# Kernel optimization log

Hardware: AMD Instinct MI355X
Metric: run time of the kernel (lower is better)

The kernel has to match this reference:

```python
import jax, jax.numpy as jnp
import numpy as np

NEAR = 0.2          # near-plane cull, matches uvd[...,2] >= 0.2 in the source
SIGMA2_MAX = 9.0    # 3-sigma disk extent, matches get_disks' sigma3 corners
ALPHA_MIN = 1.0 / 255.0


def quat_to_rot(q):
    """Unit-quaternion [P,4] (w,x,y,z) -> rotation matrices [P,3,3]."""
    q = q / (jnp.linalg.norm(q, axis=-1, keepdims=True) + 1e-12)
    w, x, y, z = q[..., 0], q[..., 1], q[..., 2], q[..., 3]
    r0 = jnp.stack([1 - 2 * (y * y + z * z), 2 * (x * y - w * z), 2 * (x * z + w * y)], -1)
    r1 = jnp.stack([2 * (x * y + w * z), 1 - 2 * (x * x + z * z), 2 * (y * z - w * x)], -1)
    r2 = jnp.stack([2 * (x * z - w * y), 2 * (y * z + w * x), 1 - 2 * (x * x + y * y)], -1)
    return jnp.stack([r0, r1, r2], -2)


def setup_inputs() -> dict:
    key = jax.random.key(0)
    k = jax.random.split(key, 6)
    H = W = 128
    P = 4096
    tanfov = 0.4
    f = W / (2.0 * tanfov)
    xs = (jnp.arange(W, dtype=jnp.float32) - (W - 1) / 2.0) / f
    ys = (jnp.arange(H, dtype=jnp.float32) - (H - 1) / 2.0) / f
    gx, gy = jnp.meshgrid(xs, ys, indexing='xy')
    d = jnp.stack([gx, gy, jnp.ones_like(gx)], -1)
    ray_d = d / jnp.linalg.norm(d, axis=-1, keepdims=True)   # [H,W,3]
    ray_o = jnp.zeros((H, W, 3), jnp.float32)
    means3D = jax.random.normal(k[0], (P, 3), jnp.float32) * 1.5 + jnp.array([0.0, 0.0, 4.0], jnp.float32)
    scales = jax.random.uniform(k[1], (P, 2), jnp.float32, 0.02, 0.15)
    rotations = jax.random.normal(k[2], (P, 4), jnp.float32)
    opacities = jax.random.uniform(k[3], (P, 1), jnp.float32, 0.3, 1.0)
    colors = jax.random.uniform(k[4], (P, 3), jnp.float32)
    bg_color = jnp.zeros((3,), jnp.float32)
    return dict(ray_o=ray_o, ray_d=ray_d, means3D=means3D, scales=scales,
                rotations=rotations, opacities=opacities, colors=colors, bg_color=bg_color)


def reference(ray_o, ray_d, means3D, scales, rotations, opacities, colors, bg_color):
    """Gaussian-surfel ray tracing: ray/disk-plane intersection, 2D Gaussian
    falloff in the surfel tangent frame, front-to-back alpha compositing in
    depth order (the math the BVH-accelerated SurfelTracer computes)."""
    H, W, _ = ray_o.shape
    ro = ray_o.reshape(-1, 3)
    rd = ray_d.reshape(-1, 3)
    R = quat_to_rot(rotations)                     # [P,3,3]
    tu, tv, nrm = R[..., :, 0], R[..., :, 1], R[..., :, 2]  # tangent frame columns

    # ray-plane intersection t = dot(mu - o, n) / dot(d, n)  -> [Nr,P]
    den = rd @ nrm.T
    num = jnp.einsum('pk,pk->p', means3D, nrm)[None, :] - ro @ nrm.T
    safe_den = jnp.where(jnp.abs(den) < 1e-8, 1e-8, den)
    t = num / safe_den

    # local disk coords u,v of hit point without materializing [Nr,P,3]
    u = (ro @ tu.T - jnp.einsum('pk,pk->p', means3D, tu)[None, :] + t * (rd @ tu.T)) / scales[None, :, 0]
    v = (ro @ tv.T - jnp.einsum('pk,pk->p', means3D, tv)[None, :] + t * (rd @ tv.T)) / scales[None, :, 1]
    r2 = u * u + v * v
    G = jnp.exp(-0.5 * r2)
    alpha = jnp.clip(opacities[None, :, 0] * G, 0.0, 0.99)
    valid = (t > NEAR) & (r2 < SIGMA2_MAX) & (jnp.abs(den) > 1e-8) & (alpha > ALPHA_MIN)
    alpha = jnp.where(valid, alpha, 0.0)

    # front-to-back compositing: sort hits by depth per ray
    t_key = jnp.where(valid, t, jnp.inf)
    order = jnp.argsort(t_key, axis=1)
    alpha_s = jnp.take_along_axis(alpha, order, axis=1)
    trans = jnp.cumprod(1.0 - alpha_s, axis=1)
    trans = jnp.concatenate([jnp.ones_like(trans[:, :1]), trans[:, :-1]], axis=1)  # exclusive
    w_s = alpha_s * trans
    inv = jnp.argsort(order, axis=1)
    w = jnp.take_along_axis(w_s, inv, axis=1)      # weights in original surfel order

    acc = w.sum(-1)                                # [Nr]
    rgb = w @ colors + (1.0 - acc)[:, None] * bg_color[None, :]
    dpt = (w * jnp.where(valid, t, 0.0)).sum(-1)
    norm = w @ nrm
    return (rgb.reshape(H, W, 3), dpt.reshape(H, W, 1),
            acc.reshape(H, W, 1), norm.reshape(H, W, 3))
```

## Files before the change

kernel.cpp:

```cpp
#include <hip/hip_runtime.h>
#include <stdint.h>

#define NEAR_T  0.2f
#define SIG2MAX 9.0f
#define AMIN    (1.0f/255.0f)
#define NSL     8
#define TS      8
#define TB      16
#define KFIX    64

__device__ __forceinline__ float dot3(float ax,float ay,float az,
                                      float bx,float by,float bz){
  return fmaf(ax,bx, fmaf(ay,by, az*bz));
}

__device__ __forceinline__ bool eval_hit(const float* __restrict__ gp,
    float rox,float roy,float roz, float rdx,float rdy,float rdz,
    float& t_out, float& a_out)
{
  float nx=gp[6], ny=gp[7], nz=gp[8];
  float den  = dot3(rdx,rdy,rdz, nx,ny,nz);
  float aden = fabsf(den);
  float num  = gp[11] - dot3(rox,roy,roz, nx,ny,nz);
  float sden = (aden < 1e-8f) ? 1e-8f : den;
  float t = __fdividef(num, sden);
  float ru = dot3(rox,roy,roz, gp[0],gp[1],gp[2]);
  float du = dot3(rdx,rdy,rdz, gp[0],gp[1],gp[2]);
  float u  = fmaf(t, du, ru - gp[9])  * gp[12];
  float rv = dot3(rox,roy,roz, gp[3],gp[4],gp[5]);
  float dv = dot3(rdx,rdy,rdz, gp[3],gp[4],gp[5]);
  float v  = fmaf(t, dv, rv - gp[10]) * gp[13];
  float r2 = fmaf(u,u, v*v);
  float G  = __expf(-0.5f*r2);
  float a  = fminf(gp[14]*G, 0.99f);
  t_out = t; a_out = a;
  return (t > NEAR_T) & (r2 < SIG2MAX) & (aden > 1e-8f) & (a > AMIN);
}

__device__ __forceinline__ unsigned long long make_key(float t, float a, uint32_t g){
  uint32_t a16 = (uint32_t)(a * 65535.f + 0.5f);
  return ((unsigned long long)__float_as_uint(t) << 32) |
         ((unsigned long long)a16 << 16) | (unsigned long long)g;
}

__device__ __forceinline__ bool pix_bbox_vals(
    float mx, float my, float mz, float ex, float ey, float ez,
    float axm, float bxm, float aym, float bym, int W, int H,
    int& x0, int& x1, int& y0, int& y1)
{
  float zmin=mz-ez, zmax=mz+ez;
  if (zmax <= 0.16f) return false;
  if (zmin <= 1e-3f){ x0=0; x1=W-1; y0=0; y1=H-1; return true; }
  float xmin=mx-ex, xmax=mx+ex, ymin=my-ey, ymax=my+ey;
  float gxmin = (xmin>=0.f)? xmin/zmax : xmin/zmin;
  float gxmax = (xmax>=0.f)? xmax/zmin : xmax/zmax;
  float gymin = (ymin>=0.f)? ymin/zmax : ymin/zmin;
  float gymax = (ymax>=0.f)? ymax/zmin : ymax/zmax;
  float p0 = (gxmin - bxm)/axm, p1 = (gxmax - bxm)/axm;
  float q0 = (gymin - bym)/aym, q1 = (gymax - bym)/aym;
  int ix0 = (int)floorf(fminf(p0,p1)) - 1;
  int ix1 = (int)ceilf (fmaxf(p0,p1)) + 1;
  int iy0 = (int)floorf(fminf(q0,q1)) - 1;
  int iy1 = (int)ceilf (fmaxf(q0,q1)) + 1;
  if (ix1 < 0 || ix0 > W-1 || iy1 < 0 || iy0 > H-1) return false;
  x0 = max(ix0,0); x1 = min(ix1,W-1);
  y0 = max(iy0,0); y1 = min(iy1,H-1);
  return true;
}

__global__ __launch_bounds__(256)
void k_prep(const float* __restrict__ rot, const float* __restrict__ means,
            const float* __restrict__ scales, const float* __restrict__ opac,
            const float* __restrict__ colors, const float* __restrict__ ray_o,
            const float* __restrict__ ray_d,
            float* __restrict__ geo, float* __restrict__ col,
            int4* __restrict__ bbox, uint32_t* __restrict__ cnt,
            uint32_t* __restrict__ badArr, int P, int npix, int W, int H)
{
  __shared__ int sBad;
  int lt = threadIdx.x;
  if (lt == 0) sBad = 0;
  __syncthreads();
  int tid = blockIdx.x*blockDim.x + lt;
  float g0x = ray_d[0]/ray_d[2], g0y = ray_d[1]/ray_d[2];
  float axm = ray_d[3]/ray_d[5] - g0x;
  float aym = ray_d[(size_t)W*3+1]/ray_d[(size_t)W*3+2] - g0y;
  bool mapok = (fabsf(axm) > 1e-12f) && (fabsf(aym) > 1e-12f);
  if (!mapok) sBad = 1;
  if (tid < npix){
    cnt[tid] = 0u;
    int ix = tid % W, iy = tid / W;
    float rox=ray_o[tid*3+0], roy=ray_o[tid*3+1], roz=ray_o[tid*3+2];
    float rdx=ray_d[tid*3+0], rdy=ray_d[tid*3+1], rdz=ray_d[tid*3+2];
    bool ok = (rox==0.f) & (roy==0.f) & (roz==0.f) & (rdz > 0.8f);
    if (ok && mapok){
      float gx = rdx/rdz, gy = rdy/rdz;
      ok = (fabsf(gx - fmaf(axm,(float)ix,g0x)) <= 3e-4f) &
           (fabsf(gy - fmaf(aym,(float)iy,g0y)) <= 3e-4f);
    }
    if (!ok) sBad = 1;
  }
  if (tid < P){
    int g = tid;
    float qw=rot[g*4+0], qx=rot[g*4+1], qy=rot[g*4+2], qz=rot[g*4+3];
    float n = sqrtf(qw*qw+qx*qx+qy*qy+qz*qz) + 1e-12f;
    qw/=n; qx/=n; qy/=n; qz/=n;
    float tux = 1.f-2.f*(qy*qy+qz*qz), tuy = 2.f*(qx*qy+qw*qz), tuz = 2.f*(qx*qz-qw*qy);
    float tvx = 2.f*(qx*qy-qw*qz), tvy = 1.f-2.f*(qx*qx+qz*qz), tvz = 2.f*(qy*qz+qw*qx);
    float nx  = 2.f*(qx*qz+qw*qy), ny  = 2.f*(qy*qz-qw*qx), nz  = 1.f-2.f*(qx*qx+qy*qy);
    float mx=means[g*3+0], my=means[g*3+1], mz=means[g*3+2];
    float sx=scales[g*2+0], sy=scales[g*2+1];
    float* gp = &geo[(size_t)g*16];
    gp[0]=tux; gp[1]=tuy; gp[2]=tuz;
    gp[3]=tvx; gp[4]=tvy; gp[5]=tvz;
    gp[6]=nx;  gp[7]=ny;  gp[8]=nz;
    gp[9]  = mx*tux+my*tuy+mz*tuz;
    gp[10] = mx*tvx+my*tvy+mz*tvz;
    gp[11] = mx*nx +my*ny +mz*nz;
    gp[12] = 1.f/sx;
    gp[13] = 1.f/sy;
    gp[14] = opac[g];
    gp[15] = 0.f;
    col[g*3+0]=colors[g*3+0]; col[g*3+1]=colors[g*3+1]; col[g*3+2]=colors[g*3+2];
    const float R3 = 3.02f;
    float ex = R3*(sx*fabsf(tux)+sy*fabsf(tvx));
    float ey = R3*(sx*fabsf(tuy)+sy*fabsf(tvy));
    float ez = R3*(sx*fabsf(tuz)+sy*fabsf(tvz));
    int x0,x1,y0,y1;
    bool ok = mapok && pix_bbox_vals(mx,my,mz, ex,ey,ez, axm,g0x,aym,g0y, W,H,
                                     x0,x1,y0,y1);
    bbox[g] = ok ? make_int4(x0,x1,y0,y1) : make_int4(1,0,1,0);
  }
  __syncthreads();
  if (lt == 0) badArr[blockIdx.x] = (uint32_t)sBad;
}

__global__ __launch_bounds__(1024)
void k_bin(int4* __restrict__ bbox, uint32_t* __restrict__ tileLen,
           uint32_t* __restrict__ tileList, const uint32_t* __restrict__ badArr,
           int nb, int P, int W, int H, int TXB, int TYB)
{
  __shared__ uint32_t sCnt[1024];
  __shared__ int sFB;
  int NTB = TXB*TYB;
  int tid = threadIdx.x;
  if (tid == 0) sFB = 0;
  for (int i=tid; i<NTB; i+=1024) sCnt[i]=0u;
  __syncthreads();
  if (tid < nb && badArr[tid] != 0u) sFB = 1;
  __syncthreads();
  if (sFB){
    for (int g=tid; g<P; g+=1024) bbox[g] = make_int4(0,W-1,0,H-1);
    __syncthreads();
  }
  for (int g=tid; g<P; g+=1024){
    int4 bb = bbox[g];
    if (bb.x > bb.y) continue;
    int tx0=bb.x/TB, tx1=bb.y/TB, ty0=bb.z/TB, ty1=bb.w/TB;
    for (int ty=ty0; ty<=ty1; ++ty)
      for (int tx=tx0; tx<=tx1; ++tx){
        int t = ty*TXB+tx;
        uint32_t slot = atomicAdd(&sCnt[t], 1u);
        tileList[(size_t)t*P + slot] = (uint32_t)g;
      }
  }
  __syncthreads();
  for (int i=tid; i<NTB; i+=1024) tileLen[i] = sCnt[i];
}

__global__ __launch_bounds__(1024)
void k_fbfix(int4* __restrict__ bbox, const uint32_t* __restrict__ badArr,
             int nb, int P, int W, int H)
{
  __shared__ int sFB;
  int tid = threadIdx.x;
  if (tid == 0) sFB = 0;
  __syncthreads();
  if (tid < nb && badArr[tid] != 0u) sFB = 1;
  __syncthreads();
  if (sFB)
    for (int g=tid; g<P; g+=1024) bbox[g] = make_int4(0,W-1,0,H-1);
}

__global__ void k_bin_global(const int4* __restrict__ bbox, uint32_t* __restrict__ tileLen,
                             uint32_t* __restrict__ tileList, int P, int TXB)
{
  int g = blockIdx.x*blockDim.x + threadIdx.x;
  if (g >= P) return;
  int4 bb = bbox[g];
  if (bb.x > bb.y) return;
  int tx0=bb.x/TB, tx1=bb.y/TB, ty0=bb.z/TB, ty1=bb.w/TB;
  for (int ty=ty0; ty<=ty1; ++ty)
    for (int tx=tx0; tx<=tx1; ++tx){
      int t = ty*TXB+tx;
      uint32_t slot = atomicAdd(&tileLen[t], 1u);
      tileList[(size_t)t*P + slot] = (uint32_t)g;
    }
}

__global__ __launch_bounds__(64)
void k_trace(const float* __restrict__ geo, const int4* __restrict__ bbox,
             const float* __restrict__ ray_o, const float* __restrict__ ray_d,
             const uint32_t* __restrict__ tileLen, const uint32_t* __restrict__ tileList,
             uint32_t* __restrict__ cnt, unsigned long long* __restrict__ keys64,
             int W, int H, int TXB, int STX, int P)
{
  int st = blockIdx.x;
  int stx = st % STX, sty = st / STX;
  int lane = threadIdx.x;
  int ix = stx*TS + (lane & (TS-1));
  int iy = sty*TS + (lane / TS);
  bool live = (ix < W) & (iy < H);
  int px = live ? (iy*W + ix) : 0;
  int pt = (sty*TS/TB)*TXB + (stx*TS/TB);
  uint32_t base = (uint32_t)pt * (uint32_t)P;
  uint32_t len  = tileLen[pt];
  int sx0 = stx*TS, sx1 = sx0 + TS-1;
  int sy0 = sty*TS, sy1 = sy0 + TS-1;
  float rox=ray_o[px*3+0], roy=ray_o[px*3+1], roz=ray_o[px*3+2];
  float rdx=ray_d[px*3+0], rdy=ray_d[px*3+1], rdz=ray_d[px*3+2];
  for (uint32_t s = blockIdx.y; s < len; s += NSL){
    int gu = __builtin_amdgcn_readfirstlane((int)tileList[base+s]);
    int4 bb = bbox[gu];
    if (bb.x > sx1 || bb.y < sx0 || bb.z > sy1 || bb.w < sy0) continue;
    const float* gp = &geo[(size_t)gu*16];
    float t,a;
    bool hit = eval_hit(gp, rox,roy,roz, rdx,rdy,rdz, t, a) && live;
    if (hit){
      uint32_t slot = atomicAdd(&cnt[px], 1u);
      if (slot < KFIX) keys64[(size_t)px*KFIX + slot] = make_key(t, a, (uint32_t)gu);
    }
  }
}

__device__ __forceinline__ float wred(float v){
  #pragma unroll
  for (int d=32; d>0; d>>=1) v += __shfl_down(v, d);
  return v;
}

__device__ __forceinline__ void comp_write(int px, int npix, int lane,
    float r_, float g_, float bl_, float dpt_, float acc_,
    float nx_, float ny_, float nz_, const float* __restrict__ bg,
    float* __restrict__ out)
{
  r_ = wred(r_); g_ = wred(g_); bl_ = wred(bl_);
  dpt_ = wred(dpt_); acc_ = wred(acc_);
  nx_ = wred(nx_); ny_ = wred(ny_); nz_ = wred(nz_);
  if (lane == 0){
    float one_m = 1.f - acc_;
    out[(size_t)px*3+0] = r_  + one_m*bg[0];
    out[(size_t)px*3+1] = g_  + one_m*bg[1];
    out[(size_t)px*3+2] = bl_ + one_m*bg[2];
    out[(size_t)npix*3 + px] = dpt_;
    out[(size_t)npix*4 + px] = acc_;
    out[(size_t)npix*5 + (size_t)px*3+0] = nx_;
    out[(size_t)npix*5 + (size_t)px*3+1] = ny_;
    out[(size_t)npix*5 + (size_t)px*3+2] = nz_;
  }
}

__global__ __launch_bounds__(256)
void k_comp_small(const unsigned long long* __restrict__ keys64,
                  const uint32_t* __restrict__ cnt,
                  const float* __restrict__ geo, const float* __restrict__ col,
                  const float* __restrict__ bg, float* __restrict__ out, int npix)
{
  int lane = threadIdx.x & 63;
  int wave = threadIdx.x >> 6;
  for (int px = (int)(blockIdx.x*4u + wave); px < npix; px += (int)(gridDim.x*4u)){
    uint32_t K = cnt[px];
    if (K > (uint32_t)KFIX) continue;
    unsigned long long key = (lane < (int)K) ? keys64[(size_t)px*KFIX + lane] : ~0ull;
    #pragma unroll
    for (int k=2; k<=64; k<<=1){
      #pragma unroll
      for (int j=k>>1; j>0; j>>=1){
        unsigned long long other = __shfl_xor(key, j);
        bool keep_min = (((lane & j) == 0) == ((lane & k) == 0));
        unsigned long long lo = key < other ? key : other;
        unsigned long long hi = key < other ? other : key;
        key = keep_min ? lo : hi;
      }
    }
    bool valid = lane < (int)K;
    const float inv65535 = 1.f/65535.f;
    float a = (float)((uint32_t)(key >> 16) & 0xFFFFu) * inv65535;
    float p = valid ? (1.f - a) : 1.f;
    float ip = p;
    #pragma unroll
    for (int d=1; d<64; d<<=1){ float v = __shfl_up(ip, d); if (lane >= d) ip *= v; }
    float T = __shfl_up(ip, 1);
    if (lane == 0) T = 1.f;
    float r_=0.f, g_=0.f, bl_=0.f, dpt_=0.f, acc_=0.f, nx_=0.f, ny_=0.f, nz_=0.f;
    if (valid){
      float t = __uint_as_float((uint32_t)(key >> 32));
      uint32_t g = (uint32_t)(key & 0xFFFFu);
      float w = a * T;
      const float* gp = &geo[(size_t)g*16];
      const float* cp = &col[(size_t)g*3];
      r_ = w*cp[0]; g_ = w*cp[1]; bl_ = w*cp[2];
      dpt_ = w*t; acc_ = w;
      nx_ = w*gp[6]; ny_ = w*gp[7]; nz_ = w*gp[8];
    }
    comp_write(px, npix, lane, r_,g_,bl_,dpt_,acc_,nx_,ny_,nz_, bg, out);
  }
}

__global__ __launch_bounds__(64)
void k_comp_over(const float* __restrict__ geo, const int4* __restrict__ bbox,
                 const float* __restrict__ col,
                 const float* __restrict__ ray_o, const float* __restrict__ ray_d,
                 const uint32_t* __restrict__ tileLen, const uint32_t* __restrict__ tileList,
                 const uint32_t* __restrict__ cnt, const float* __restrict__ bg,
                 float* __restrict__ out, int npix, int W, int TXB, int P)
{
  __shared__ unsigned long long sk[4096];
  int lane = threadIdx.x;
  unsigned long long lt = (1ull << lane) - 1ull;
  for (int px = (int)blockIdx.x; px < npix; px += (int)gridDim.x){
    if (cnt[px] <= (uint32_t)KFIX) continue;
    int ix = px % W, iy = px / W;
    int pt = (iy/TB)*TXB + (ix/TB);
    uint32_t base = (uint32_t)pt * (uint32_t)P;
    uint32_t len  = tileLen[pt];
    float rox=ray_o[px*3+0], roy=ray_o[px*3+1], roz=ray_o[px*3+2];
    float rdx=ray_d[px*3+0], rdy=ray_d[px*3+1], rdz=ray_d[px*3+2];

    uint32_t run = 0;
    for (uint32_t s0=0; s0<len; s0+=64){
      uint32_t s = s0 + (uint32_t)lane;
      bool act = s < len;
      uint32_t gu = act ? tileList[base+s] : 0u;
      float t=0.f, a=0.f;
      bool hit = false;
      if (act){
        int4 bb = bbox[gu];
        if (bb.x <= ix && ix <= bb.y && bb.z <= iy && iy <= bb.w)
          hit = eval_hit(&geo[(size_t)gu*16], rox,roy,roz, rdx,rdy,rdz, t, a);
      }
      unsigned long long m = __ballot(hit);
      if (hit){
        uint32_t slot = run + (uint32_t)__popcll(m & lt);
        if (slot < 4096u) sk[slot] = make_key(t, a, gu);
      }
      run += (uint32_t)__popcll(m);
    }
    uint32_t K = min(run, 4096u);
    uint32_t N = 1; while (N < K) N <<= 1;
    for (uint32_t i=K+lane; i<N; i+=64) sk[i] = ~0ull;
    __syncthreads();

    for (uint32_t kk=2; kk<=N; kk<<=1){
      for (uint32_t j=kk>>1; j>0; j>>=1){
        for (uint32_t i=lane; i<N; i+=64){
          uint32_t ij = i ^ j;
          if (ij > i){
            unsigned long long a = sk[i], b = sk[ij];
            bool up = ((i & kk) == 0);
            if ((a > b) == up){ sk[i] = b; sk[ij] = a; }
          }
        }
        __syncthreads();
      }
    }

    const float inv65535 = 1.f/65535.f;
    uint32_t C = (K + 63) >> 6;
    uint32_t b0 = lane*C, e0 = min(b0 + C, K);
    float p = 1.f;
    for (uint32_t i=b0; i<e0; ++i){
      float a = (float)((uint32_t)(sk[i] >> 16) & 0xFFFFu) * inv65535;
      p *= (1.f - a);
    }
    float ip = p;
    #pragma unroll
    for (int d=1; d<64; d<<=1){ float v = __shfl_up(ip, d); if (lane >= d) ip *= v; }
    float T = __shfl_up(ip, 1);
    if (lane == 0) T = 1.f;

    float r_=0.f, g_=0.f, bl_=0.f, dpt_=0.f, acc_=0.f, nx_=0.f, ny_=0.f, nz_=0.f;
    for (uint32_t i=b0; i<e0; ++i){
      unsigned long long key = sk[i];
      float t = __uint_as_float((uint32_t)(key >> 32));
      float a = (float)((uint32_t)(key >> 16) & 0xFFFFu) * inv65535;
      uint32_t g = (uint32_t)(key & 0xFFFFu);
      float w = a * T;
      const float* gp = &geo[(size_t)g*16];
      const float* cp = &col[(size_t)g*3];
      r_  += w * cp[0]; g_ += w * cp[1]; bl_ += w * cp[2];
      dpt_ += w * t; acc_ += w;
      nx_ += w * gp[6]; ny_ += w * gp[7]; nz_ += w * gp[8];
      T *= (1.f - a);
    }
    comp_write(px, npix, lane, r_,g_,bl_,dpt_,acc_,nx_,ny_,nz_, bg, out);
    __syncthreads();
  }
}

extern "C" void kernel_launch(void* const* d_in, const int* in_sizes, int n_in,
                              void* d_out, int out_size, void* d_ws, size_t ws_size,
                              hipStream_t stream)
{
  const float* ray_o  = (const float*)d_in[0];
  const float* ray_d  = (const float*)d_in[1];
  const float* means  = (const float*)d_in[2];
  const float* scales = (const float*)d_in[3];
  const float* rot    = (const float*)d_in[4];
  const float* opac   = (const float*)d_in[5];
  const float* colors = (const float*)d_in[6];
  const float* bg     = (const float*)d_in[7];
  float* out = (float*)d_out;

  int npix = in_sizes[0] / 3;
  int P    = in_sizes[2] / 3;
  int W    = (int)(sqrtf((float)npix) + 0.5f);
  int H    = npix / W;
  int TXB  = (W + TB - 1) / TB;
  int TYB  = (H + TB - 1) / TB;
  int NTB  = TXB * TYB;
  int STX  = (W + TS - 1) / TS;
  int STY  = (H + TS - 1) / TS;
  int NST  = STX * STY;

  int initN = npix > P ? npix : P;
  int nPrepBlocks = (initN + 255)/256;

  uint8_t* ws = (uint8_t*)d_ws;
  size_t o_geo   = 0;
  size_t sz_geo  = ((size_t)P*16*4 + 255) & ~(size_t)255;
  size_t o_col   = o_geo + sz_geo;
  size_t sz_col  = ((size_t)P*3*4 + 255) & ~(size_t)255;
  size_t o_bbox  = o_col + sz_col;
  size_t sz_bbox = ((size_t)P*16 + 255) & ~(size_t)255;
  size_t o_cnt   = o_bbox + sz_bbox;
  size_t sz_pix  = ((size_t)npix*4 + 255) & ~(size_t)255;
  size_t o_tlen  = o_cnt + sz_pix;
  size_t sz_ntb  = ((size_t)NTB*4 + 255) & ~(size_t)255;
  size_t o_bad   = o_tlen + sz_ntb;
  size_t sz_bad  = ((size_t)nPrepBlocks*4 + 255) & ~(size_t)255;
  size_t o_tlist = o_bad + sz_bad;
  size_t sz_tlist= (((size_t)NTB*(size_t)P*4) + 255) & ~(size_t)255;
  size_t o_k64   = o_tlist + sz_tlist;

  float*    geo     = (float*)(ws + o_geo);
  float*    col     = (float*)(ws + o_col);
  int4*     bbox    = (int4*)(ws + o_bbox);
  uint32_t* cnt     = (uint32_t*)(ws + o_cnt);
  uint32_t* tileLen = (uint32_t*)(ws + o_tlen);
  uint32_t* badArr  = (uint32_t*)(ws + o_bad);
  uint32_t* tileList= (uint32_t*)(ws + o_tlist);
  unsigned long long* keys64 = (unsigned long long*)(ws + o_k64);

  k_prep<<<nPrepBlocks, 256, 0, stream>>>(rot, means, scales, opac, colors,
                                          ray_o, ray_d, geo, col, bbox, cnt,
                                          badArr, P, npix, W, H);
  if (NTB <= 1024){
    k_bin<<<1, 1024, 0, stream>>>(bbox, tileLen, tileList, badArr, nPrepBlocks,
                                  P, W, H, TXB, TYB);
  } else {
    k_fbfix<<<1, 1024, 0, stream>>>(bbox, badArr, nPrepBlocks, P, W, H);
    hipMemsetAsync(tileLen, 0, sz_ntb, stream);
    k_bin_global<<<(P + 255)/256, 256, 0, stream>>>(bbox, tileLen, tileList, P, TXB);
  }
  dim3 tgrid(NST, NSL);
  k_trace<<<tgrid, 64, 0, stream>>>(geo, bbox, ray_o, ray_d, tileLen, tileList,
                                    cnt, keys64, W, H, TXB, STX, P);
  k_comp_small<<<1024, 256, 0, stream>>>(keys64, cnt, geo, col, bg, out, npix);
  k_comp_over<<<1024, 64, 0, stream>>>(geo, bbox, col, ray_o, ray_d, tileLen, tileList,
                                       cnt, bg, out, npix, W, TXB, P);
}
```

Baseline: 132.6 us.

## Bin gaussians per tile in parallel blocks and merge compositing kernels

Replaces the single-block binning kernel, which loops over every gaussian with shared atomics across all tiles, with one block per tile. Each block scans all gaussians against its own tile bbox, and a fallback flag replaces the old step that rewrote bbox. The small-count and overflow compositing kernels are merged into one launch, with the overflow path run by wave 0 of each block, which removes its block barriers. This cuts launches and the serial binning bottleneck, at the cost of every tile block reading every bbox and the overflow path using only a quarter of each block's threads.

Result: faster. 121.7 us (-8.2%).

```diff
diff --git a/kernel.cpp b/kernel.cpp
--- a/kernel.cpp
+++ b/kernel.cpp
@@ -135,74 +135,43 @@
   if (lt == 0) badArr[blockIdx.x] = (uint32_t)sBad;
 }
 
-__global__ __launch_bounds__(1024)
-void k_bin(int4* __restrict__ bbox, uint32_t* __restrict__ tileLen,
-           uint32_t* __restrict__ tileList, const uint32_t* __restrict__ badArr,
-           int nb, int P, int W, int H, int TXB, int TYB)
-{
-  __shared__ uint32_t sCnt[1024];
+__global__ __launch_bounds__(256)
+void k_bin_tile(const int4* __restrict__ bbox, uint32_t* __restrict__ tileLen,
+                uint32_t* __restrict__ tileList, const uint32_t* __restrict__ badArr,
+                uint32_t* __restrict__ fbFlag, int nb, int P, int TXB)
+{
+  __shared__ uint32_t sCnt;
   __shared__ int sFB;
-  int NTB = TXB*TYB;
+  int t = blockIdx.x;
   int tid = threadIdx.x;
-  if (tid == 0) sFB = 0;
-  for (int i=tid; i<NTB; i+=1024) sCnt[i]=0u;
+  if (tid == 0){ sCnt = 0u; sFB = 0; }
   __syncthreads();
-  if (tid < nb && badArr[tid] != 0u) sFB = 1;
+  for (int i=tid; i<nb; i+=256) if (badArr[i] != 0u) sFB = 1;
   __syncthreads();
-  if (sFB){
-    for (int g=tid; g<P; g+=1024) bbox[g] = make_int4(0,W-1,0,H-1);
-    __syncthreads();
-  }
-  for (int g=tid; g<P; g+=1024){
+  bool fb = (sFB != 0);
+  if (t == 0 && tid == 0) fbFlag[0] = fb ? 1u : 0u;
+  int tx = t % TXB, ty = t / TXB;
+  int x0t = tx*TB, x1t = x0t + TB-1;
+  int y0t = ty*TB, y1t = y0t + TB-1;
+  for (int g=tid; g<P; g+=256){
     int4 bb = bbox[g];
-    if (bb.x > bb.y) continue;
-    int tx0=bb.x/TB, tx1=bb.y/TB, ty0=bb.z/TB, ty1=bb.w/TB;
-    for (int ty=ty0; ty<=ty1; ++ty)
-      for (int tx=tx0; tx<=tx1; ++tx){
-        int t = ty*TXB+tx;
-        uint32_t slot = atomicAdd(&sCnt[t], 1u);
-        tileList[(size_t)t*P + slot] = (uint32_t)g;
-      }
+    bool match = fb || ((bb.x <= bb.y) &&
+                 !(bb.x > x1t || bb.y < x0t || bb.z > y1t || bb.w < y0t));
+    if (match){
+      uint32_t slot = atomicAdd(&sCnt, 1u);
+      tileList[(size_t)t*P + slot] = (uint32_t)g;
+    }
   }
   __syncthreads();
-  for (int i=tid; i<NTB; i+=1024) tileLen[i] = sCnt[i];
-}
-
-__global__ __launch_bounds__(1024)
-void k_fbfix(int4* __restrict__ bbox, const uint32_t* __restrict__ badArr,
-             int nb, int P, int W, int H)
-{
-  __shared__ int sFB;
-  int tid = threadIdx.x;
-  if (tid == 0) sFB = 0;
-  __syncthreads();
-  if (tid < nb && badArr[tid] != 0u) sFB = 1;
-  __syncthreads();
-  if (sFB)
-    for (int g=tid; g<P; g+=1024) bbox[g] = make_int4(0,W-1,0,H-1);
-}
-
-__global__ void k_bin_global(const int4* __restrict__ bbox, uint32_t* __restrict__ tileLen,
-                             uint32_t* __restrict__ tileList, int P, int TXB)
-{
-  int g = blockIdx.x*blockDim.x + threadIdx.x;
-  if (g >= P) return;
-  int4 bb = bbox[g];
-  if (bb.x > bb.y) return;
-  int tx0=bb.x/TB, tx1=bb.y/TB, ty0=bb.z/TB, ty1=bb.w/TB;
-  for (int ty=ty0; ty<=ty1; ++ty)
-    for (int tx=tx0; tx<=tx1; ++tx){
-      int t = ty*TXB+tx;
-      uint32_t slot = atomicAdd(&tileLen[t], 1u);
-      tileList[(size_t)t*P + slot] = (uint32_t)g;
-    }
+  if (tid == 0) tileLen[t] = sCnt;
 }
 
 __global__ __launch_bounds__(64)
 void k_trace(const float* __restrict__ geo, const int4* __restrict__ bbox,
              const float* __restrict__ ray_o, const float* __restrict__ ray_d,
              const uint32_t* __restrict__ tileLen, const uint32_t* __restrict__ tileList,
-             uint32_t* __restrict__ cnt, unsigned long long* __restrict__ keys64,
+             const uint32_t* __restrict__ fbFlag, uint32_t* __restrict__ cnt,
+             unsigned long long* __restrict__ keys64,
              int W, int H, int TXB, int STX, int P)
 {
   int st = blockIdx.x;
@@ -215,14 +184,17 @@
   int pt = (sty*TS/TB)*TXB + (stx*TS/TB);
   uint32_t base = (uint32_t)pt * (uint32_t)P;
   uint32_t len  = tileLen[pt];
+  bool fb = (fbFlag[0] != 0u);
   int sx0 = stx*TS, sx1 = sx0 + TS-1;
   int sy0 = sty*TS, sy1 = sy0 + TS-1;
   float rox=ray_o[px*3+0], roy=ray_o[px*3+1], roz=ray_o[px*3+2];
   float rdx=ray_d[px*3+0], rdy=ray_d[px*3+1], rdz=ray_d[px*3+2];
   for (uint32_t s = blockIdx.y; s < len; s += NSL){
     int gu = __builtin_amdgcn_readfirstlane((int)tileList[base+s]);
-    int4 bb = bbox[gu];
-    if (bb.x > sx1 || bb.y < sx0 || bb.z > sy1 || bb.w < sy0) continue;
+    if (!fb){
+      int4 bb = bbox[gu];
+      if (bb.x > sx1 || bb.y < sx0 || bb.z > sy1 || bb.w < sy0) continue;
+    }
     const float* gp = &geo[(size_t)gu*16];
     float t,a;
     bool hit = eval_hit(gp, rox,roy,roz, rdx,rdy,rdz, t, a) && live;
@@ -261,13 +233,20 @@
 }
 
 __global__ __launch_bounds__(256)
-void k_comp_small(const unsigned long long* __restrict__ keys64,
-                  const uint32_t* __restrict__ cnt,
-                  const float* __restrict__ geo, const float* __restrict__ col,
-                  const float* __restrict__ bg, float* __restrict__ out, int npix)
-{
+void k_comp(const unsigned long long* __restrict__ keys64,
+            const uint32_t* __restrict__ cnt,
+            const float* __restrict__ geo, const int4* __restrict__ bbox,
+            const float* __restrict__ col,
+            const float* __restrict__ ray_o, const float* __restrict__ ray_d,
+            const uint32_t* __restrict__ tileLen, const uint32_t* __restrict__ tileList,
+            const uint32_t* __restrict__ fbFlag, const float* __restrict__ bg,
+            float* __restrict__ out, int npix, int W, int TXB, int P)
+{
+  __shared__ unsigned long long sk[4096];
   int lane = threadIdx.x & 63;
   int wave = threadIdx.x >> 6;
+  const float inv65535 = 1.f/65535.f;
+
   for (int px = (int)(blockIdx.x*4u + wave); px < npix; px += (int)(gridDim.x*4u)){
     uint32_t K = cnt[px];
     if (K > (uint32_t)KFIX) continue;
@@ -284,7 +263,6 @@
       }
     }
     bool valid = lane < (int)K;
-    const float inv65535 = 1.f/65535.f;
     float a = (float)((uint32_t)(key >> 16) & 0xFFFFu) * inv65535;
     float p = valid ? (1.f - a) : 1.f;
     float ip = p;
@@ -305,19 +283,10 @@
     }
     comp_write(px, npix, lane, r_,g_,bl_,dpt_,acc_,nx_,ny_,nz_, bg, out);
   }
-}
-
-__global__ __launch_bounds__(64)
-void k_comp_over(const float* __restrict__ geo, const int4* __restrict__ bbox,
-                 const float* __restrict__ col,
-                 const float* __restrict__ ray_o, const float* __restrict__ ray_d,
-                 const uint32_t* __restrict__ tileLen, const uint32_t* __restrict__ tileList,
-                 const uint32_t* __restrict__ cnt, const float* __restrict__ bg,
-                 float* __restrict__ out, int npix, int W, int TXB, int P)
-{
-  __shared__ unsigned long long sk[4096];
-  int lane = threadIdx.x;
-  unsigned long long lt = (1ull << lane) - 1ull;
+
+  if (wave != 0) return;
+  bool fb = (fbFlag[0] != 0u);
+  unsigned long long ltm = (1ull << lane) - 1ull;
   for (int px = (int)blockIdx.x; px < npix; px += (int)gridDim.x){
     if (cnt[px] <= (uint32_t)KFIX) continue;
     int ix = px % W, iy = px / W;
@@ -336,12 +305,12 @@
       bool hit = false;
       if (act){
         int4 bb = bbox[gu];
-        if (bb.x <= ix && ix <= bb.y && bb.z <= iy && iy <= bb.w)
+        if (fb || (bb.x <= ix && ix <= bb.y && bb.z <= iy && iy <= bb.w))
           hit = eval_hit(&geo[(size_t)gu*16], rox,roy,roz, rdx,rdy,rdz, t, a);
       }
       unsigned long long m = __ballot(hit);
       if (hit){
-        uint32_t slot = run + (uint32_t)__popcll(m & lt);
+        uint32_t slot = run + (uint32_t)__popcll(m & ltm);
         if (slot < 4096u) sk[slot] = make_key(t, a, gu);
       }
       run += (uint32_t)__popcll(m);
@@ -349,7 +318,6 @@
     uint32_t K = min(run, 4096u);
     uint32_t N = 1; while (N < K) N <<= 1;
     for (uint32_t i=K+lane; i<N; i+=64) sk[i] = ~0ull;
-    __syncthreads();
 
     for (uint32_t kk=2; kk<=N; kk<<=1){
       for (uint32_t j=kk>>1; j>0; j>>=1){
@@ -361,11 +329,9 @@
             if ((a > b) == up){ sk[i] = b; sk[ij] = a; }
           }
         }
-        __syncthreads();
       }
     }
 
-    const float inv65535 = 1.f/65535.f;
     uint32_t C = (K + 63) >> 6;
     uint32_t b0 = lane*C, e0 = min(b0 + C, K);
     float p = 1.f;
@@ -394,7 +360,6 @@
       T *= (1.f - a);
     }
     comp_write(px, npix, lane, r_,g_,bl_,dpt_,acc_,nx_,ny_,nz_, bg, out);
-    __syncthreads();
   }
 }
 
@@ -437,7 +402,8 @@
   size_t sz_pix  = ((size_t)npix*4 + 255) & ~(size_t)255;
   size_t o_tlen  = o_cnt + sz_pix;
   size_t sz_ntb  = ((size_t)NTB*4 + 255) & ~(size_t)255;
-  size_t o_bad   = o_tlen + sz_ntb;
+  size_t o_fb    = o_tlen + sz_ntb;
+  size_t o_bad   = o_fb + 256;
   size_t sz_bad  = ((size_t)nPrepBlocks*4 + 255) & ~(size_t)255;
   size_t o_tlist = o_bad + sz_bad;
   size_t sz_tlist= (((size_t)NTB*(size_t)P*4) + 255) & ~(size_t)255;
@@ -448,6 +414,7 @@
   int4*     bbox    = (int4*)(ws + o_bbox);
   uint32_t* cnt     = (uint32_t*)(ws + o_cnt);
   uint32_t* tileLen = (uint32_t*)(ws + o_tlen);
+  uint32_t* fbFlag  = (uint32_t*)(ws + o_fb);
   uint32_t* badArr  = (uint32_t*)(ws + o_bad);
   uint32_t* tileList= (uint32_t*)(ws + o_tlist);
   unsigned long long* keys64 = (unsigned long long*)(ws + o_k64);
@@ -455,18 +422,12 @@
   k_prep<<<nPrepBlocks, 256, 0, stream>>>(rot, means, scales, opac, colors,
                                           ray_o, ray_d, geo, col, bbox, cnt,
                                           badArr, P, npix, W, H);
-  if (NTB <= 1024){
-    k_bin<<<1, 1024, 0, stream>>>(bbox, tileLen, tileList, badArr, nPrepBlocks,
-                                  P, W, H, TXB, TYB);
-  } else {
-    k_fbfix<<<1, 1024, 0, stream>>>(bbox, badArr, nPrepBlocks, P, W, H);
-    hipMemsetAsync(tileLen, 0, sz_ntb, stream);
-    k_bin_global<<<(P + 255)/256, 256, 0, stream>>>(bbox, tileLen, tileList, P, TXB);
-  }
+  k_bin_tile<<<NTB, 256, 0, stream>>>(bbox, tileLen, tileList, badArr, fbFlag,
+                                      nPrepBlocks, P, TXB);
   dim3 tgrid(NST, NSL);
   k_trace<<<tgrid, 64, 0, stream>>>(geo, bbox, ray_o, ray_d, tileLen, tileList,
-                                    cnt, keys64, W, H, TXB, STX, P);
-  k_comp_small<<<1024, 256, 0, stream>>>(keys64, cnt, geo, col, bg, out, npix);
-  k_comp_over<<<1024, 64, 0, stream>>>(geo, bbox, col, ray_o, ray_d, tileLen, tileList,
-                                       cnt, bg, out, npix, W, TXB, P);
-}
+                                    fbFlag, cnt, keys64, W, H, TXB, STX, P);
+  k_comp<<<1024, 256, 0, stream>>>(keys64, cnt, geo, bbox, col, ray_o, ray_d,
+                                   tileLen, tileList, fbFlag, bg, out,
+                                   npix, W, TXB, P);
+}
```
